# Performance work log

Measured on AMD Instinct MI355X. Metric: run time of the kernel, lower is better.

Reference implementation:

```python
import jax, jax.numpy as jnp
import numpy as np

BITS = 4
GROUPSIZE = 128
IN_FEATURES = 4096
OUT_FEATURES = 4096
GROUPS = IN_FEATURES // GROUPSIZE  # 32
TOKENS = 8192


def setup_inputs() -> dict:
    key = jax.random.key(0)
    k_x, k_s, k_b = jax.random.split(key, 3)
    rng = np.random.default_rng(0)
    # packed 4-bit weights: 8 nibbles per int32 word
    qweight = jnp.asarray(
        rng.integers(-2**31, 2**31, size=(IN_FEATURES // 8, OUT_FEATURES), dtype=np.int64).astype(np.int32)
    )
    qzeros = jnp.asarray(
        rng.integers(-2**31, 2**31, size=(GROUPS, OUT_FEATURES // 8), dtype=np.int64).astype(np.int32)
    )
    scales = jax.random.uniform(k_s, (GROUPS, OUT_FEATURES), dtype=jnp.float32) * 0.02 + 0.001
    g_idx = (jnp.arange(IN_FEATURES, dtype=jnp.int32) // GROUPSIZE).astype(jnp.int32)
    bias = jax.random.normal(k_b, (OUT_FEATURES,), dtype=jnp.float32) * 0.01
    x = jax.random.normal(k_x, (TOKENS, IN_FEATURES), dtype=jnp.float32)
    return {"x": x, "qweight": qweight, "qzeros": qzeros, "scales": scales,
            "g_idx": g_idx, "bias": bias}


def reference(x, qweight, qzeros, scales, g_idx, bias):
    out_features = qweight.shape[1]
    in_features = qweight.shape[0] * 8
    mask = jnp.int32(15)  # 2**bits - 1
    wf = jnp.arange(0, 32, BITS, dtype=jnp.int32)  # [8] nibble shift amounts
    # unpack zero points: [groups, out//8, 8] -> [groups, out]
    zeros = ((qzeros[:, :, None] >> wf[None, None, :]) & mask) + 1
    zeros = zeros.reshape(scales.shape)
    # unpack weights: [in//8, 8, out] -> [in, out]
    weight = (qweight[:, None, :] >> wf[None, :, None]) & mask
    weight = weight.reshape(in_features, out_features)
    # dequantize per group and matmul
    W = scales[g_idx] * (weight - zeros[g_idx]).astype(scales.dtype)
    out = x @ W
    return out + bias
```

## Files before the change

kernel.cpp:

```cpp
#include <hip/hip_runtime.h>
#include <cstdint>
#include <cstddef>

#define IN_F   4096
#define OUT_F  4096
#define NTOK   8192
#define NGRP   32

#define BM 128
#define BN 128
#define BK 32

typedef __attribute__((ext_vector_type(8))) __bf16 bf16x8;
typedef __attribute__((ext_vector_type(4))) float  floatx4;

__device__ __forceinline__ unsigned short f2bf(float f) {
    unsigned int u = __builtin_bit_cast(unsigned int, f);
    u += 0x7fffu + ((u >> 16) & 1u);
    return (unsigned short)(u >> 16);
}

__device__ __forceinline__ void gload16(const void* g, void* l) {
    __builtin_amdgcn_global_load_lds(
        (const __attribute__((address_space(1))) void*)g,
        (__attribute__((address_space(3))) void*)l,
        16, 0, 0);
}

__global__ void dequant_kernel(const int* __restrict__ qweight,
                               const int* __restrict__ qzeros,
                               const float* __restrict__ scales,
                               const int* __restrict__ g_idx,
                               unsigned short* __restrict__ Wt) {
    const int t  = blockIdx.x * 256 + threadIdx.x;
    const int n  = t >> 9;
    const int k8 = t & 511;
    const int k  = k8 * 8;

    const int g  = g_idx[k];
    const int qw = qweight[(size_t)k8 * OUT_F + n];
    const int zw = qzeros[g * (OUT_F / 8) + (n >> 3)];
    const int z  = ((zw >> (4 * (n & 7))) & 15) + 1;
    const float s = scales[g * OUT_F + n];
    const float sz = s * (float)z;

    union { unsigned short h[8]; uint4 v; } u;
#pragma unroll
    for (int j = 0; j < 8; ++j) {
        const int q = (qw >> (4 * j)) & 15;
        u.h[j] = f2bf(s * (float)q - sz);
    }
    *(uint4*)(Wt + (size_t)n * IN_F + k) = u.v;
}

__global__ void xcast_kernel(const float* __restrict__ x,
                             unsigned short* __restrict__ Xb) {
    const size_t i = ((size_t)blockIdx.x * 256 + threadIdx.x) * 8;
    const float4 a = *(const float4*)(x + i);
    const float4 b = *(const float4*)(x + i + 4);
    union { unsigned short h[8]; uint4 v; } u;
    u.h[0] = f2bf(a.x); u.h[1] = f2bf(a.y); u.h[2] = f2bf(a.z); u.h[3] = f2bf(a.w);
    u.h[4] = f2bf(b.x); u.h[5] = f2bf(b.y); u.h[6] = f2bf(b.z); u.h[7] = f2bf(b.w);
    *(uint4*)(Xb + i) = u.v;
}

__global__ void gemm_kernel(const unsigned short* __restrict__ Xb,
                            const unsigned short* __restrict__ Wt,
                            const float* __restrict__ bias,
                            float* __restrict__ out) {
    __shared__ unsigned short As[BM * BK];
    __shared__ unsigned short Bs[BN * BK];

    const int tid  = threadIdx.x;
    const int wave = tid >> 6;
    const int lane = tid & 63;
    const int wm   = (wave >> 1) * 64;
    const int wn   = (wave & 1) * 64;
    const int m0   = blockIdx.y * BM;
    const int n0   = blockIdx.x * BN;

    const int sr = lane >> 2;
    const int sc = lane & 3;

    const int mi = lane & 15;
    const int kq = lane >> 4;

    floatx4 acc[4][4];
#pragma unroll
    for (int i = 0; i < 4; ++i)
#pragma unroll
        for (int j = 0; j < 4; ++j)
            acc[i][j] = floatx4{0.f, 0.f, 0.f, 0.f};

    const unsigned short* Ag = Xb + (size_t)m0 * IN_F;
    const unsigned short* Bg = Wt + (size_t)n0 * IN_F;

    for (int k0 = 0; k0 < IN_F; k0 += BK) {
        __syncthreads();
#pragma unroll
        for (int c = 0; c < 2; ++c) {
            const int q   = wave * 2 + c;
            const int row = q * 16 + sr;
            gload16(Ag + (size_t)row * IN_F + k0 + sc * 8, (void*)(As + q * 16 * BK));
            gload16(Bg + (size_t)row * IN_F + k0 + sc * 8, (void*)(Bs + q * 16 * BK));
        }
        __syncthreads();

        bf16x8 av[4], bv[4];
#pragma unroll
        for (int i = 0; i < 4; ++i)
            av[i] = *(const bf16x8*)(As + (wm + i * 16 + mi) * BK + kq * 8);
#pragma unroll
        for (int j = 0; j < 4; ++j)
            bv[j] = *(const bf16x8*)(Bs + (wn + j * 16 + mi) * BK + kq * 8);
#pragma unroll
        for (int i = 0; i < 4; ++i)
#pragma unroll
            for (int j = 0; j < 4; ++j)
                acc[i][j] = __builtin_amdgcn_mfma_f32_16x16x32_bf16(
                    av[i], bv[j], acc[i][j], 0, 0, 0);
    }

    const int mq = lane >> 4;
#pragma unroll
    for (int j = 0; j < 4; ++j) {
        const int col = n0 + wn + j * 16 + mi;
        const float bb = bias[col];
#pragma unroll
        for (int i = 0; i < 4; ++i) {
#pragma unroll
            for (int r = 0; r < 4; ++r) {
                const int row = m0 + wm + i * 16 + mq * 4 + r;
                out[(size_t)row * OUT_F + col] = acc[i][j][r] + bb;
            }
        }
    }
}

extern "C" void kernel_launch(void* const* d_in, const int* in_sizes, int n_in,
                              void* d_out, int out_size, void* d_ws, size_t ws_size,
                              hipStream_t stream) {
    const float* x       = (const float*)d_in[0];
    const int*   qweight = (const int*)d_in[1];
    const int*   qzeros  = (const int*)d_in[2];
    const float* scales  = (const float*)d_in[3];
    const int*   g_idx   = (const int*)d_in[4];
    const float* bias    = (const float*)d_in[5];
    float*       out     = (float*)d_out;

    unsigned short* Wt = (unsigned short*)d_ws;
    unsigned short* Xb = Wt + (size_t)OUT_F * IN_F;

    dequant_kernel<<<(OUT_F * (IN_F / 8)) / 256, 256, 0, stream>>>(
        qweight, qzeros, scales, g_idx, Wt);
    xcast_kernel<<<((size_t)NTOK * IN_F / 8) / 256, 256, 0, stream>>>(x, Xb);

    dim3 grid(OUT_F / BN, NTOK / BM);
    gemm_kernel<<<grid, 256, 0, stream>>>(Xb, Wt, bias, out);
}
```

Measured before the change: 555.7 us.

## Coalesce dequant writes via LDS transpose and swizzle GEMM LDS tiles

The dequant kernel now has each thread handle eight k-chunks for a single output column, so qweight reads are coalesced across n. Results are staged in a swizzled shared-memory tile and written to Wt as contiguous 128-byte row segments. The GEMM applies an XOR swizzle to the chunk index when it loads global data into LDS and when it reads fragments back, to cut LDS bank conflicts on the MFMA operand reads. This adds extra index arithmetic and a block barrier in dequant, and the two swizzles must stay consistent or the results will be wrong.

Measured after the change: 545.6 us. No clear change (-1.8%).

```diff
diff --git a/kernel.cpp b/kernel.cpp
--- a/kernel.cpp
+++ b/kernel.cpp
@@ -32,25 +32,36 @@
                                const float* __restrict__ scales,
                                const int* __restrict__ g_idx,
                                unsigned short* __restrict__ Wt) {
-    const int t  = blockIdx.x * 256 + threadIdx.x;
-    const int n  = t >> 9;
-    const int k8 = t & 511;
-    const int k  = k8 * 8;
+    __shared__ unsigned short tile[256 * 64];
+    const int tk  = blockIdx.x & 63;
+    const int tn  = blockIdx.x >> 6;
+    const int tid = threadIdx.x;
+    const int n   = tn * 256 + tid;
 
-    const int g  = g_idx[k];
-    const int qw = qweight[(size_t)k8 * OUT_F + n];
-    const int zw = qzeros[g * (OUT_F / 8) + (n >> 3)];
-    const int z  = ((zw >> (4 * (n & 7))) & 15) + 1;
-    const float s = scales[g * OUT_F + n];
-    const float sz = s * (float)z;
-
-    union { unsigned short h[8]; uint4 v; } u;
 #pragma unroll
-    for (int j = 0; j < 8; ++j) {
-        const int q = (qw >> (4 * j)) & 15;
-        u.h[j] = f2bf(s * (float)q - sz);
+    for (int r = 0; r < 8; ++r) {
+        const int k8 = tk * 8 + r;
+        const int k  = k8 * 8;
+        const int g  = g_idx[k];
+        const int qw = qweight[(size_t)k8 * OUT_F + n];
+        const float s = scales[g * OUT_F + n];
+        const int  zw = qzeros[g * (OUT_F / 8) + (n >> 3)];
+        const float z = (float)(((zw >> (4 * (n & 7))) & 15) + 1);
+        const float sz = s * z;
+        union { unsigned short h[8]; uint4 v; } u;
+#pragma unroll
+        for (int j = 0; j < 8; ++j)
+            u.h[j] = f2bf(s * (float)((qw >> (4 * j)) & 15) - sz);
+        *(uint4*)(tile + tid * 64 + ((r ^ (tid & 7)) * 8)) = u.v;
     }
-    *(uint4*)(Wt + (size_t)n * IN_F + k) = u.v;
+    __syncthreads();
+#pragma unroll
+    for (int i = 0; i < 8; ++i) {
+        const int nl = i * 32 + (tid >> 3);
+        const int c  = tid & 7;
+        const uint4 v = *(const uint4*)(tile + nl * 64 + ((c ^ (nl & 7)) * 8));
+        *(uint4*)(Wt + (size_t)(tn * 256 + nl) * IN_F + tk * 64 + c * 8) = v;
+    }
 }
 
 __global__ void xcast_kernel(const float* __restrict__ x,
@@ -79,11 +90,13 @@
     const int m0   = blockIdx.y * BM;
     const int n0   = blockIdx.x * BN;
 
-    const int sr = lane >> 2;
-    const int sc = lane & 3;
+    const int sr   = lane >> 2;
+    const int sc   = lane & 3;
+    const int gch  = sc ^ ((sr >> 1) & 3);
 
     const int mi = lane & 15;
     const int kq = lane >> 4;
+    const int swz = (mi >> 1) & 3;
 
     floatx4 acc[4][4];
 #pragma unroll
@@ -101,18 +114,18 @@
         for (int c = 0; c < 2; ++c) {
             const int q   = wave * 2 + c;
             const int row = q * 16 + sr;
-            gload16(Ag + (size_t)row * IN_F + k0 + sc * 8, (void*)(As + q * 16 * BK));
-            gload16(Bg + (size_t)row * IN_F + k0 + sc * 8, (void*)(Bs + q * 16 * BK));
+            gload16(Ag + (size_t)row * IN_F + k0 + gch * 8, (void*)(As + q * 16 * BK));
+            gload16(Bg + (size_t)row * IN_F + k0 + gch * 8, (void*)(Bs + q * 16 * BK));
         }
         __syncthreads();
 
         bf16x8 av[4], bv[4];
 #pragma unroll
         for (int i = 0; i < 4; ++i)
-            av[i] = *(const bf16x8*)(As + (wm + i * 16 + mi) * BK + kq * 8);
+            av[i] = *(const bf16x8*)(As + (wm + i * 16 + mi) * BK + ((kq ^ swz) * 8));
 #pragma unroll
         for (int j = 0; j < 4; ++j)
-            bv[j] = *(const bf16x8*)(Bs + (wn + j * 16 + mi) * BK + kq * 8);
+            bv[j] = *(const bf16x8*)(Bs + (wn + j * 16 + mi) * BK + ((kq ^ swz) * 8));
 #pragma unroll
         for (int i = 0; i < 4; ++i)
 #pragma unroll
@@ -151,8 +164,7 @@
     unsigned short* Wt = (unsigned short*)d_ws;
     unsigned short* Xb = Wt + (size_t)OUT_F * IN_F;
 
-    dequant_kernel<<<(OUT_F * (IN_F / 8)) / 256, 256, 0, stream>>>(
-        qweight, qzeros, scales, g_idx, Wt);
+    dequant_kernel<<<64 * 16, 256, 0, stream>>>(qweight, qzeros, scales, g_idx, Wt);
     xcast_kernel<<<((size_t)NTOK * IN_F / 8) / 256, 256, 0, stream>>>(x, Xb);
 
     dim3 grid(OUT_F / BN, NTOK / BM);
```
